# Performance work log

Hardware: AMD Instinct MI355X
Metric: run time of the kernel (lower is better)

## Reference

```python
import jax, jax.numpy as jnp
import numpy as np

N = 50000      # nodes
E = 800000     # edges
T = 3          # npass
ED = 64        # embedding_dim
NS = 23        # nshifts (arange(0.8, 3.0+1e-5, 0.1))
MD = NS + ED   # message_dim = 87
H = 200        # hidden width (hardcoded in module)
NMOL = 2048    # number of molecules (segments for final scatter)
RD = ED * (T + 1)  # readout input dim = 256
EPS = 1e-5

SHIFTS = jnp.asarray(np.arange(0.8, 3.0 + 1e-5, 0.1, dtype=np.float32))  # [23]


def setup_inputs() -> dict:
    key = jax.random.key(0)
    ks = jax.random.split(key, 32)
    inp = {
        'z_i': jax.random.randint(ks[0], (N,), 0, 10),
        'edge_index': jax.random.randint(ks[1], (2, E), 0, N),
        'dist_ij': jax.random.uniform(ks[2], (E, 1), dtype=jnp.float32) * 2.2 + 0.8,
        'mol_ind': jnp.sort(jax.random.randint(ks[3], (N,), 0, NMOL)),
        'emb': jax.random.normal(ks[4], (10, ED), dtype=jnp.float32),
        # per-pass update MLP params, stacked over T
        'up_bn_g': jnp.ones((T, MD), jnp.float32),
        'up_bn_b': jnp.zeros((T, MD), jnp.float32),
        'up_w1': jax.random.normal(ks[5], (T, MD, H), jnp.float32) * 0.05,
        'up_b1': jnp.zeros((T, H), jnp.float32),
        'up_w2': jax.random.normal(ks[6], (T, H, H), jnp.float32) * 0.05,
        'up_b2': jnp.zeros((T, H), jnp.float32),
        'up_w3': jax.random.normal(ks[7], (T, H, H), jnp.float32) * 0.05,
        'up_b3': jnp.zeros((T, H), jnp.float32),
        'up_w4': jax.random.normal(ks[8], (T, H, ED), jnp.float32) * 0.05,
        'up_b4': jnp.zeros((T, ED), jnp.float32),
        # readout MLP params
        'ro_bn_g': jnp.ones((RD,), jnp.float32),
        'ro_bn_b': jnp.zeros((RD,), jnp.float32),
        'ro_w1': jax.random.normal(ks[9], (RD, H), jnp.float32) * 0.05,
        'ro_b1': jnp.zeros((H,), jnp.float32),
        'ro_w2': jax.random.normal(ks[10], (H, H), jnp.float32) * 0.05,
        'ro_b2': jnp.zeros((H,), jnp.float32),
        'ro_w3': jax.random.normal(ks[11], (H, H), jnp.float32) * 0.05,
        'ro_b3': jnp.zeros((H,), jnp.float32),
        'ro_w4': jax.random.normal(ks[12], (H, 1), jnp.float32) * 0.05,
        'ro_b4': jnp.zeros((1,), jnp.float32),  # bias filled to 0 in __init__
    }
    return inp


def batchnorm(x, g, b):
    # BatchNorm1d in training mode: batch statistics, biased variance
    mu = jnp.mean(x, axis=0)
    var = jnp.mean(jnp.square(x - mu), axis=0)
    return (x - mu) * jax.lax.rsqrt(var + EPS) * g + b


def mlp(x, g, b, w1, b1, w2, b2, w3, b3, w4, b4):
    x = batchnorm(x, g, b)
    x = jax.nn.relu(x @ w1 + b1)
    x = jax.nn.relu(x @ w2 + b2)
    x = jax.nn.relu(x @ w3 + b3)
    return x @ w4 + b4


def reference(z_i, edge_index, dist_ij, mol_ind, emb,
              up_bn_g, up_bn_b, up_w1, up_b1, up_w2, up_b2, up_w3, up_b3, up_w4, up_b4,
              ro_bn_g, ro_bn_b, ro_w1, ro_b1, ro_w2, ro_b2, ro_w3, ro_b3, ro_w4, ro_b4):
    e_source, e_sink = edge_index[0], edge_index[1]
    rbf_ij = jnp.exp(-jnp.square(dist_ij - SHIFTS[None, :]))  # [E, NS]
    x_i = emb[z_i]                                            # [N, ED]
    x_list = [x_i]
    for t in range(T):
        m_ij = jnp.concatenate([rbf_ij, x_i[e_sink]], axis=1)  # [E, MD] gather
        m_i = jax.ops.segment_sum(m_ij, e_source, num_segments=N)  # scatter-sum
        x_i = x_i + 0.1 * mlp(m_i, up_bn_g[t], up_bn_b[t],
                              up_w1[t], up_b1[t], up_w2[t], up_b2[t],
                              up_w3[t], up_b3[t], up_w4[t], up_b4[t])
        x_list.append(x_i)
    x_all = jnp.concatenate(x_list, axis=1)  # [N, RD]
    y_i = mlp(x_all, ro_bn_g, ro_bn_b, ro_w1, ro_b1, ro_w2, ro_b2, ro_w3, ro_b3, ro_w4, ro_b4)
    y = jax.ops.segment_sum(y_i, mol_ind, num_segments=NMOL)  # [NMOL, 1]
    return y
```

## Files before the change

kernel.cpp:

```cpp
#include <hip/hip_runtime.h>
#include <hip/hip_bf16.h>
#include <type_traits>

#define NN 50000
#define NP 50048
#define EE 800000
#define TT 3
#define ED 64
#define NS 23
#define MD 87
#define HH 200
#define NMOL 2048
#define RD 256

#define SW 216
#define NPB2 512
#define SNB ((NN + 255) / 256)

typedef __attribute__((ext_vector_type(8))) short short8b;
typedef __attribute__((ext_vector_type(4))) float f32x4;

__device__ __forceinline__ unsigned short f2bf(float f) {
  unsigned u = __float_as_uint(f);
  return (unsigned short)((u + 0x7fffu + ((u >> 16) & 1u)) >> 16);
}
__device__ __forceinline__ float ubf2f(unsigned short h) {
  return __uint_as_float(((unsigned)h) << 16);
}
__device__ __forceinline__ float bfp2f(unsigned p) {
  return __uint_as_float(p << 16) + __uint_as_float(p & 0xffff0000u);
}
__device__ __forceinline__ unsigned packsplit(float v) {
  unsigned short h = f2bf(v);
  unsigned short l = f2bf(v - ubf2f(h));
  return (unsigned)h | ((unsigned)l << 16);
}

__device__ __forceinline__ void gl2lds16(const short* g, short* l) {
  __builtin_amdgcn_global_load_lds(
      (const __attribute__((address_space(1))) unsigned int*)g,
      (__attribute__((address_space(3))) unsigned int*)l, 16, 0, 0);
}

struct WD { const float* src; short* dst; int K, N, Kpad, Npad, T; };
struct WDs { WD d[5]; };

__global__ __launch_bounds__(256) void wprep_kernel(WDs W) {
  WD w = W.d[blockIdx.y];
  int KB = w.Kpad >> 5, NT = w.Npad >> 4;
  int per = w.Npad * w.Kpad;
  int total = w.T * per;
  for (int idx = blockIdx.x * 256 + threadIdx.x; idx < total; idx += gridDim.x * 256) {
    int t = idx / per;
    int r = idx - t * per;
    int e = r & 7, lane = (r >> 3) & 63;
    int blk = r >> 9;
    int kb = blk % KB, tile = blk / KB;
    int ln = lane & 15, quad = lane >> 4;
    int n = tile * 16 + ln, k = kb * 32 + quad * 8 + e;
    float v = 0.f;
    if (k < w.K && n < w.N) v = w.src[((size_t)t * w.K + k) * w.N + n];
    unsigned short h = f2bf(v);
    unsigned short l = f2bf(v - ubf2f(h));
    size_t base = ((size_t)(t * NT + tile) * KB + kb) * 1024;
    w.dst[base + lane * 8 + e] = (short)h;
    w.dst[base + 512 + lane * 8 + e] = (short)l;
  }
}

__global__ __launch_bounds__(256) void wscale_kernel(const float* __restrict__ wsrc,
                                                     const float* __restrict__ na,
                                                     const float* __restrict__ nb,
                                                     const float* __restrict__ bsrc,
                                                     int K, int Kpad,
                                                     short* __restrict__ wsp,
                                                     float* __restrict__ bc) {
  int n = blockIdx.x;
  int k = threadIdx.x;
  int KB = Kpad >> 5;
  int tile = n >> 4, ln = n & 15;
  float contrib = 0.f;
  if (k < Kpad) {
    float v = 0.f;
    if (n < HH && k < K) {
      float w = wsrc[(size_t)k * HH + n];
      v = na[k] * w;
      contrib = nb[k] * w;
    }
    unsigned short h = f2bf(v);
    unsigned short l = f2bf(v - ubf2f(h));
    int kb = k >> 5, quad = (k & 31) >> 3, e = k & 7;
    int lane = quad * 16 + ln;
    size_t base = ((size_t)tile * KB + kb) * 1024;
    wsp[base + lane * 8 + e] = (short)h;
    wsp[base + 512 + lane * 8 + e] = (short)l;
  }
  __shared__ float sh[256];
  sh[k] = contrib;
  __syncthreads();
  for (int off = 128; off > 0; off >>= 1) {
    if (k < off) sh[k] += sh[k + off];
    __syncthreads();
  }
  if (k == 0) bc[n] = (n < HH ? bsrc[n] : 0.f) + sh[0];
}

__global__ __launch_bounds__(256) void emb_kernel(const int* __restrict__ z,
                                                  const float* __restrict__ emb,
                                                  unsigned* __restrict__ xp,
                                                  short* __restrict__ xq,
                                                  short* __restrict__ xqs) {
  int idx = blockIdx.x * 256 + threadIdx.x;
  if (idx >= NN * ED) return;
  int i = idx >> 6, d = idx & 63;
  unsigned pk = packsplit(emb[z[i] * ED + d]);
  xp[(size_t)i * RD + d] = pk;
  short h = (short)(pk & 0xffffu);
  xq[(size_t)i * RD + d] = h;
  xqs[(size_t)i * ED + d] = h;
}

__global__ __launch_bounds__(256) void hist_kernel(const int* __restrict__ src,
                                                   int* __restrict__ deg) {
  int e = blockIdx.x * 256 + threadIdx.x;
  if (e < EE) atomicAdd(&deg[src[e]], 1);
}

__global__ __launch_bounds__(256) void scanA_kernel(const int* __restrict__ deg,
                                                    int* __restrict__ Psum) {
  int i = blockIdx.x * 256 + threadIdx.x;
  int v = (i < NN) ? deg[i] : 0;
#pragma unroll
  for (int off = 32; off > 0; off >>= 1) v += __shfl_down(v, off, 64);
  __shared__ int ws[4];
  if ((threadIdx.x & 63) == 0) ws[threadIdx.x >> 6] = v;
  __syncthreads();
  if (threadIdx.x == 0) Psum[blockIdx.x] = ws[0] + ws[1] + ws[2] + ws[3];
}

__global__ __launch_bounds__(256) void scanB_kernel(const int* __restrict__ Psum,
                                                    int* __restrict__ Poff) {
  __shared__ int sh[256];
  int t = threadIdx.x;
  int v = (t < SNB) ? Psum[t] : 0;
  sh[t] = v;
  __syncthreads();
  for (int off = 1; off < 256; off <<= 1) {
    int u = (t >= off) ? sh[t - off] : 0;
    __syncthreads();
    sh[t] += u;
    __syncthreads();
  }
  if (t < SNB) Poff[t] = sh[t] - v;
}

__global__ __launch_bounds__(256) void scanC_kernel(const int* __restrict__ deg,
                                                    const int* __restrict__ Poff,
                                                    int* __restrict__ offs,
                                                    int* __restrict__ cursor) {
  __shared__ int sh[256];
  int t = threadIdx.x;
  int i = blockIdx.x * 256 + t;
  int v = (i < NN) ? deg[i] : 0;
  sh[t] = v;
  __syncthreads();
  for (int off = 1; off < 256; off <<= 1) {
    int u = (t >= off) ? sh[t - off] : 0;
    __syncthreads();
    sh[t] += u;
    __syncthreads();
  }
  int excl = Poff[blockIdx.x] + sh[t] - v;
  if (i < NN) {
    offs[i] = excl;
    cursor[i] = excl;
    if (i == NN - 1) offs[NN] = excl + v;
  }
}

__global__ __launch_bounds__(256) void scatter_kernel(const int* __restrict__ src,
                                                      const int* __restrict__ snk,
                                                      const float* __restrict__ dist,
                                                      int* __restrict__ cursor,
                                                      int* __restrict__ ssink,
                                                      float* __restrict__ sdist) {
  int e = blockIdx.x * 256 + threadIdx.x;
  if (e >= EE) return;
  int p = atomicAdd(&cursor[src[e]], 1);
  ssink[p] = snk[e];
  sdist[p] = dist[e];
}

template <bool RBF>
__global__ __launch_bounds__(256) void gather_kernel(const int* __restrict__ offs,
                                                     const int* __restrict__ ssink,
                                                     const float* __restrict__ sdist,
                                                     const short* __restrict__ xqs,
                                                     short* __restrict__ mh) {
  int node = blockIdx.x * 4 + (threadIdx.x >> 6);
  int lane = threadIdx.x & 63;
  if (node >= NN) return;
  float shift = (float)(0.8 + 0.1 * (double)lane);
  int e0 = offs[node], e1 = offs[node + 1];
  float ax0 = 0.f, ax1 = 0.f, ar0 = 0.f, ar1 = 0.f;
  int j = e0;
  for (; j + 4 <= e1; j += 4) {
    int s0 = ssink[j], s1 = ssink[j + 1], s2 = ssink[j + 2], s3 = ssink[j + 3];
    float x0 = ubf2f((unsigned short)xqs[(size_t)s0 * ED + lane]);
    float x1 = ubf2f((unsigned short)xqs[(size_t)s1 * ED + lane]);
    float x2 = ubf2f((unsigned short)xqs[(size_t)s2 * ED + lane]);
    float x3 = ubf2f((unsigned short)xqs[(size_t)s3 * ED + lane]);
    ax0 += x0 + x2;
    ax1 += x1 + x3;
    if (RBF && lane < NS) {
      float d0 = sdist[j], d1 = sdist[j + 1], d2 = sdist[j + 2], d3 = sdist[j + 3];
      float u0 = d0 - shift, u1 = d1 - shift, u2 = d2 - shift, u3 = d3 - shift;
      ar0 += __expf(-u0 * u0) + __expf(-u2 * u2);
      ar1 += __expf(-u1 * u1) + __expf(-u3 * u3);
    }
  }
  for (; j < e1; j++) {
    int s = ssink[j];
    ax0 += ubf2f((unsigned short)xqs[(size_t)s * ED + lane]);
    if (RBF && lane < NS) {
      float u = sdist[j] - shift;
      ar0 += __expf(-u * u);
    }
  }
  float accx = ax0 + ax1;
  if (RBF && lane < NS) mh[(size_t)node * 96 + lane] = (short)f2bf(ar0 + ar1);
  if (RBF && lane >= NS && lane < 32) mh[(size_t)node * 96 + 64 + lane] = 0;
  mh[(size_t)node * 96 + NS + lane] = (short)f2bf(accx);
}

template <int LD>
__global__ __launch_bounds__(256) void colstats_s16_kernel(const short* __restrict__ X,
                                                           float* __restrict__ P) {
  constexpr int CG = LD / 8;
  constexpr int RPB = 256 / CG;
  const int t = threadIdx.x;
  const int cg = t % CG, rin = t / CG;
  float s[8] = {0, 0, 0, 0, 0, 0, 0, 0}, q[8] = {0, 0, 0, 0, 0, 0, 0, 0};
  if (rin < RPB) {
    for (int r = blockIdx.x * RPB + rin; r < NN; r += gridDim.x * RPB) {
      union { uint4 v; short e[8]; } u;
      u.v = *(const uint4*)(X + (size_t)r * LD + cg * 8);
#pragma unroll
      for (int e = 0; e < 8; e++) {
        float f = ubf2f((unsigned short)u.e[e]);
        s[e] += f;
        q[e] += f * f;
      }
    }
  }
  __shared__ float sh[256][16];
#pragma unroll
  for (int e = 0; e < 8; e++) { sh[t][e] = s[e]; sh[t][8 + e] = q[e]; }
  __syncthreads();
  if (rin == 0) {
    for (int rr = 1; rr < RPB; rr++) {
      const float* o = sh[rr * CG + cg];
#pragma unroll
      for (int e = 0; e < 8; e++) { s[e] += o[e]; q[e] += o[8 + e]; }
    }
    float* Pb = P + blockIdx.x * 512;
#pragma unroll
    for (int e = 0; e < 8; e++) {
      Pb[cg * 8 + e] = s[e];
      Pb[256 + cg * 8 + e] = q[e];
    }
  }
}

__global__ __launch_bounds__(256) void bnfinal2_kernel(const float* __restrict__ P, int nblk,
                                                       const float* __restrict__ g,
                                                       const float* __restrict__ b, int ncols,
                                                       float* __restrict__ na,
                                                       float* __restrict__ nb) {
  int c = blockIdx.x;
  int t = threadIdx.x;
  float s = 0.f, q = 0.f;
  for (int i = t; i < nblk; i += 256) {
    s += P[i * 512 + c];
    q += P[i * 512 + 256 + c];
  }
#pragma unroll
  for (int off = 32; off > 0; off >>= 1) {
    s += __shfl_down(s, off, 64);
    q += __shfl_down(q, off, 64);
  }
  __shared__ float ws[4], wq[4];
  if ((t & 63) == 0) { ws[t >> 6] = s; wq[t >> 6] = q; }
  __syncthreads();
  if (t == 0) {
    s = ws[0] + ws[1] + ws[2] + ws[3];
    q = wq[0] + wq[1] + wq[2] + wq[3];
    if (c < ncols) {
      float mean = s / (float)NN;
      float var = q / (float)NN - mean * mean;
      float a = g[c] * rsqrtf(var + 1e-5f);
      na[c] = a;
      nb[c] = b[c] - mean * a;
    } else {
      na[c] = 0.f;
      nb[c] = 0.f;
    }
  }
}

template <bool READOUT>
__global__ __launch_bounds__(256, 3) void fused_kernel(
    const short* __restrict__ Agh,
    const short* __restrict__ W1p, const short* __restrict__ W2p,
    const short* __restrict__ W3p, const short* __restrict__ W4p,
    const float* __restrict__ b1, const float* __restrict__ b2,
    const float* __restrict__ b3, const float* __restrict__ b4,
    unsigned* __restrict__ xp, short* __restrict__ xq, short* __restrict__ xqs,
    int t, const float* __restrict__ w4ro, const int* __restrict__ mol,
    float* __restrict__ out) {
  __shared__ short act[64 * SW];
  __shared__ short bufW[2][13 * 512];
  constexpr int GLDA = READOUT ? RD : 96;
  constexpr int KB1 = READOUT ? 8 : 3;
  const int tid = threadIdx.x;
  const int wave = tid >> 6, lane = tid & 63, ln = lane & 15, quad = lane >> 4;
  const int q8 = quad * 8;
  const int bm = blockIdx.x * 64;

  f32x4 acc[4][4];
  const short8b zfrag = {0, 0, 0, 0, 0, 0, 0, 0};

  auto stage = [&](const short* __restrict__ Wp, int NT, int KB, int TERMS,
                   int s, int b) {
    int kb = (TERMS == 2) ? (s >> 1) : s;
    int pl = (TERMS == 2) ? ((s & 1) << 9) : 0;
#pragma unroll
    for (int j = 0; j < 4; j++) {
      int tile = wave + 4 * j;
      if (tile < NT)
        gl2lds16(Wp + (size_t)(tile * KB + kb) * 1024 + pl + lane * 8,
                 &bufW[b][tile * 512]);
    }
  };

  auto runloop = [&](const short* __restrict__ AG, const short* __restrict__ Wp,
                     int NT, int KB, int TERMS) {
    const int NSL = KB * TERMS;
#pragma unroll
    for (int j = 0; j < 4; j++)
#pragma unroll
      for (int i = 0; i < 4; i++) acc[j][i] = (f32x4){0.f, 0.f, 0.f, 0.f};
    for (int s = 0; s < NSL; ++s) {
      if (s + 1 < NSL) stage(Wp, NT, KB, TERMS, s + 1, (s + 1) & 1);
      int kb = (TERMS == 2) ? (s >> 1) : s;
      short8b a[4];
      if (AG) {
#pragma unroll
        for (int i = 0; i < 4; i++)
          a[i] = *(const short8b*)(AG + (size_t)(bm + i * 16 + ln) * GLDA +
                                   kb * 32 + q8);
      } else {
        int col = kb * 32 + q8;
#pragma unroll
        for (int i = 0; i < 4; i++)
          a[i] = (col < 208) ? *(const short8b*)(act + (i * 16 + ln) * SW + col)
                             : zfrag;
      }
      const short* bw = &bufW[s & 1][0];
#pragma unroll
      for (int j = 0; j < 4; j++) {
        int tile = wave + 4 * j;
        if (tile < NT) {
          short8b b = *(const short8b*)(bw + tile * 512 + lane * 8);
#pragma unroll
          for (int i = 0; i < 4; i++)
            acc[j][i] =
                __builtin_amdgcn_mfma_f32_16x16x32_bf16(a[i], b, acc[j][i], 0, 0, 0);
        }
      }
      __syncthreads();
    }
  };

  auto epi = [&](const float* __restrict__ bias) {
#pragma unroll
    for (int j = 0; j < 4; j++) {
      int tile = wave + 4 * j;
      if (tile < 13) {
        int colg = tile * 16 + ln;
        float bb = (colg < HH) ? bias[colg] : 0.f;
#pragma unroll
        for (int i = 0; i < 4; i++)
#pragma unroll
          for (int r = 0; r < 4; r++)
            act[(i * 16 + quad * 4 + r) * SW + colg] =
                (short)f2bf(fmaxf(acc[j][i][r] + bb, 0.f));
      }
    }
  };

  stage(W1p, 13, KB1, 2, 0, 0);
  __syncthreads();
  runloop(Agh, W1p, 13, KB1, 2);
  stage(W2p, 13, 7, 1, 0, 0);
  epi(b1);
  __syncthreads();

  runloop(nullptr, W2p, 13, 7, 1);
  stage(W3p, 13, 7, 1, 0, 0);
  epi(b2);
  __syncthreads();

  runloop(nullptr, W3p, 13, 7, 1);

  if constexpr (!READOUT) {
    stage(W4p, 4, 7, 2, 0, 0);
    epi(b3);
    __syncthreads();
    runloop(nullptr, W4p, 4, 7, 2);
    int colg = wave * 16 + ln;
    float bb = b4[colg];
#pragma unroll
    for (int i = 0; i < 4; i++)
#pragma unroll
      for (int r = 0; r < 4; r++) {
        int grow = bm + i * 16 + quad * 4 + r;
        if (grow < NN) {
          size_t base = (size_t)grow * RD;
          float oldv = bfp2f(xp[base + (size_t)t * ED + colg]);
          unsigned pk = packsplit(oldv + 0.1f * (acc[0][i][r] + bb));
          xp[base + (size_t)(t + 1) * ED + colg] = pk;
          short h = (short)(pk & 0xffffu);
          xq[base + (size_t)(t + 1) * ED + colg] = h;
          xqs[(size_t)(t + 1) * NN * ED + (size_t)grow * ED + colg] = h;
        }
      }
  } else {
    epi(b3);
    __syncthreads();
    int row = tid >> 2;
    float s = 0.f;
    for (int c = (tid & 3); c < HH; c += 4)
      s += ubf2f((unsigned short)act[row * SW + c]) * w4ro[c];
    s += __shfl_xor(s, 1, 64);
    s += __shfl_xor(s, 2, 64);
    int grow = bm + row;
    if ((tid & 3) == 0 && grow < NN) atomicAdd(&out[mol[grow]], s + b4[0]);
  }
}

extern "C" void kernel_launch(void* const* d_in, const int* in_sizes, int n_in,
                              void* d_out, int out_size, void* d_ws, size_t ws_size,
                              hipStream_t stream) {
  const int* z_i = (const int*)d_in[0];
  const int* e_src = (const int*)d_in[1];
  const int* e_snk = ((const int*)d_in[1]) + EE;
  const float* dist = (const float*)d_in[2];
  const int* mol = (const int*)d_in[3];
  const float* emb = (const float*)d_in[4];
  const float* up_bn_g = (const float*)d_in[5];
  const float* up_bn_b = (const float*)d_in[6];
  const float* up_w1 = (const float*)d_in[7];
  const float* up_b1 = (const float*)d_in[8];
  const float* up_w2 = (const float*)d_in[9];
  const float* up_b2 = (const float*)d_in[10];
  const float* up_w3 = (const float*)d_in[11];
  const float* up_b3 = (const float*)d_in[12];
  const float* up_w4 = (const float*)d_in[13];
  const float* up_b4 = (const float*)d_in[14];
  const float* ro_bn_g = (const float*)d_in[15];
  const float* ro_bn_b = (const float*)d_in[16];
  const float* ro_w1 = (const float*)d_in[17];
  const float* ro_b1 = (const float*)d_in[18];
  const float* ro_w2 = (const float*)d_in[19];
  const float* ro_b2 = (const float*)d_in[20];
  const float* ro_w3 = (const float*)d_in[21];
  const float* ro_b3 = (const float*)d_in[22];
  const float* ro_w4 = (const float*)d_in[23];
  const float* ro_b4 = (const float*)d_in[24];
  float* out = (float*)d_out;

  char* p = (char*)d_ws;
  auto alloc = [&](size_t bytes) {
    void* r = (void*)p;
    p += (bytes + 255) & ~(size_t)255;
    return r;
  };
  unsigned* x_p = (unsigned*)alloc((size_t)NN * RD * 4);
  short* x_q = (short*)alloc((size_t)NP * RD * 2);
  short* x_qs = (short*)alloc((size_t)(TT + 1) * NN * ED * 2);
  short* mh = (short*)alloc((size_t)NP * 96 * 2);
  int* ssink = (int*)alloc((size_t)EE * 4);
  float* sdist = (float*)alloc((size_t)EE * 4);
  int* offs = (int*)alloc((size_t)(NN + 1) * 4);
  int* deg = (int*)alloc((size_t)NN * 4);
  int* cursor = (int*)alloc((size_t)NN * 4);
  int* Psum = (int*)alloc((size_t)SNB * 4);
  int* Poff = (int*)alloc((size_t)SNB * 4);
  float* P = (float*)alloc((size_t)NPB2 * 512 * 4);
  float* na = (float*)alloc(256 * 4);
  float* nb = (float*)alloc(256 * 4);
  float* b1c = (float*)alloc(208 * 4);
  short* w1sp = (short*)alloc((size_t)13 * 3 * 1024 * 2);
  short* r1sp = (short*)alloc((size_t)13 * 8 * 1024 * 2);
  short* w2p = (short*)alloc((size_t)TT * 13 * 7 * 1024 * 2);
  short* w3p = (short*)alloc((size_t)TT * 13 * 7 * 1024 * 2);
  short* w4p = (short*)alloc((size_t)TT * 4 * 7 * 1024 * 2);
  short* r2p = (short*)alloc((size_t)13 * 7 * 1024 * 2);
  short* r3p = (short*)alloc((size_t)13 * 7 * 1024 * 2);

  hipMemsetAsync(deg, 0, (size_t)NN * 4, stream);
  hipMemsetAsync(out, 0, (size_t)NMOL * 4, stream);

  WDs descs;
  descs.d[0] = {up_w2, w2p, HH, HH, 224, 208, TT};
  descs.d[1] = {up_w3, w3p, HH, HH, 224, 208, TT};
  descs.d[2] = {up_w4, w4p, HH, ED, 224, 64, TT};
  descs.d[3] = {ro_w2, r2p, HH, HH, 224, 208, 1};
  descs.d[4] = {ro_w3, r3p, HH, HH, 224, 208, 1};
  wprep_kernel<<<dim3(546, 5), 256, 0, stream>>>(descs);

  emb_kernel<<<(NN * ED + 255) / 256, 256, 0, stream>>>(z_i, emb, x_p, x_q, x_qs);
  hist_kernel<<<(EE + 255) / 256, 256, 0, stream>>>(e_src, deg);
  scanA_kernel<<<SNB, 256, 0, stream>>>(deg, Psum);
  scanB_kernel<<<1, 256, 0, stream>>>(Psum, Poff);
  scanC_kernel<<<SNB, 256, 0, stream>>>(deg, Poff, offs, cursor);
  scatter_kernel<<<(EE + 255) / 256, 256, 0, stream>>>(e_src, e_snk, dist, cursor, ssink, sdist);

  const int gM = NP / 64;

  for (int t = 0; t < TT; t++) {
    if (t == 0)
      gather_kernel<true><<<(NN + 3) / 4, 256, 0, stream>>>(
          offs, ssink, sdist, x_qs, mh);
    else
      gather_kernel<false><<<(NN + 3) / 4, 256, 0, stream>>>(
          offs, ssink, sdist, x_qs + (size_t)t * NN * ED, mh);
    colstats_s16_kernel<96><<<NPB2, 256, 0, stream>>>(mh, P);
    bnfinal2_kernel<<<256, 256, 0, stream>>>(P, NPB2, up_bn_g + t * MD, up_bn_b + t * MD, MD,
                                             na, nb);
    wscale_kernel<<<208, 256, 0, stream>>>(up_w1 + (size_t)t * MD * HH, na, nb,
                                           up_b1 + t * HH, MD, 96, w1sp, b1c);
    fused_kernel<false><<<gM, 256, 0, stream>>>(
        mh, w1sp,
        w2p + (size_t)t * 13 * 7 * 1024, w3p + (size_t)t * 13 * 7 * 1024,
        w4p + (size_t)t * 4 * 7 * 1024,
        b1c, up_b2 + t * HH, up_b3 + t * HH, up_b4 + t * ED,
        x_p, x_q, x_qs, t, nullptr, nullptr, nullptr);
  }

  colstats_s16_kernel<256><<<NPB2, 256, 0, stream>>>(x_q, P);
  bnfinal2_kernel<<<256, 256, 0, stream>>>(P, NPB2, ro_bn_g, ro_bn_b, RD, na, nb);
  wscale_kernel<<<208, 256, 0, stream>>>(ro_w1, na, nb, ro_b1, RD, 256, r1sp, b1c);
  fused_kernel<true><<<gM, 256, 0, stream>>>(
      x_q, r1sp, r2p, r3p, nullptr,
      b1c, ro_b2, ro_b3, ro_b4,
      nullptr, nullptr, nullptr, 0, ro_w4, mol, out);

  (void)in_sizes; (void)n_in; (void)out_size; (void)ws_size;
}
```

Measured before the change: 632.2 us.

## Hold MLP weight fragments in registers instead of double-buffered LDS staging

Each layer's packed weight fragments are now loaded directly from global memory into a per-thread register array, replacing the LDS double-buffer fed by global_load_lds and its per-k-step barriers. The fully unrolled MFMA loop reads B operands from registers, and only a few explicit barriers remain around the activation epilogues. This trades higher register pressure (launch bounds lowered from 3 to 2 blocks per CU) and redundant global weight loads per block for fewer synchronisations and less LDS traffic. Weight loads for the next layer are issued before the epilogue so they overlap with it.

```diff
diff --git a/kernel.cpp b/kernel.cpp
--- a/kernel.cpp
+++ b/kernel.cpp
@@ -20,6 +20,8 @@
 typedef __attribute__((ext_vector_type(8))) short short8b;
 typedef __attribute__((ext_vector_type(4))) float f32x4;
 
+template <int V> using ic = std::integral_constant<int, V>;
+
 __device__ __forceinline__ unsigned short f2bf(float f) {
   unsigned u = __float_as_uint(f);
   return (unsigned short)((u + 0x7fffu + ((u >> 16) & 1u)) >> 16);
@@ -34,12 +36,6 @@
   unsigned short h = f2bf(v);
   unsigned short l = f2bf(v - ubf2f(h));
   return (unsigned)h | ((unsigned)l << 16);
-}
-
-__device__ __forceinline__ void gl2lds16(const short* g, short* l) {
-  __builtin_amdgcn_global_load_lds(
-      (const __attribute__((address_space(1))) unsigned int*)g,
-      (__attribute__((address_space(3))) unsigned int*)l, 16, 0, 0);
 }
 
 struct WD { const float* src; short* dst; int K, N, Kpad, Npad, T; };
@@ -309,7 +305,7 @@
 }
 
 template <bool READOUT>
-__global__ __launch_bounds__(256, 3) void fused_kernel(
+__global__ __launch_bounds__(256, 2) void fused_kernel(
     const short* __restrict__ Agh,
     const short* __restrict__ W1p, const short* __restrict__ W2p,
     const short* __restrict__ W3p, const short* __restrict__ W4p,
@@ -319,66 +315,77 @@
     int t, const float* __restrict__ w4ro, const int* __restrict__ mol,
     float* __restrict__ out) {
   __shared__ short act[64 * SW];
-  __shared__ short bufW[2][13 * 512];
   constexpr int GLDA = READOUT ? RD : 96;
   constexpr int KB1 = READOUT ? 8 : 3;
+  constexpr int NB = READOUT ? 32 : 28;
   const int tid = threadIdx.x;
   const int wave = tid >> 6, lane = tid & 63, ln = lane & 15, quad = lane >> 4;
   const int q8 = quad * 8;
   const int bm = blockIdx.x * 64;
 
+  *(unsigned*)(act + (tid >> 2) * SW + 208 + (tid & 3) * 2) = 0u;
+
   f32x4 acc[4][4];
+  short8b Breg[NB];
   const short8b zfrag = {0, 0, 0, 0, 0, 0, 0, 0};
 
-  auto stage = [&](const short* __restrict__ Wp, int NT, int KB, int TERMS,
-                   int s, int b) {
-    int kb = (TERMS == 2) ? (s >> 1) : s;
-    int pl = (TERMS == 2) ? ((s & 1) << 9) : 0;
+  auto loadB = [&](auto slt, auto tmt, auto ntt, const short* __restrict__ Wp,
+                   int KBfull, int kb0) {
+    constexpr int SL = decltype(slt)::value;
+    constexpr int TM = decltype(tmt)::value;
+    constexpr int NT = decltype(ntt)::value;
 #pragma unroll
     for (int j = 0; j < 4; j++) {
       int tile = wave + 4 * j;
-      if (tile < NT)
-        gl2lds16(Wp + (size_t)(tile * KB + kb) * 1024 + pl + lane * 8,
-                 &bufW[b][tile * 512]);
+      if (tile < NT) {
+#pragma unroll
+        for (int s = 0; s < SL; s++) {
+          int kb = kb0 + ((TM == 2) ? (s >> 1) : s);
+          int pl = (TM == 2) ? ((s & 1) << 9) : 0;
+          Breg[j * SL + s] = *(const short8b*)(
+              Wp + (size_t)(tile * KBfull + kb) * 1024 + pl + lane * 8);
+        }
+      }
     }
   };
 
-  auto runloop = [&](const short* __restrict__ AG, const short* __restrict__ Wp,
-                     int NT, int KB, int TERMS) {
-    const int NSL = KB * TERMS;
-#pragma unroll
-    for (int j = 0; j < 4; j++)
-#pragma unroll
-      for (int i = 0; i < 4; i++) acc[j][i] = (f32x4){0.f, 0.f, 0.f, 0.f};
-    for (int s = 0; s < NSL; ++s) {
-      if (s + 1 < NSL) stage(Wp, NT, KB, TERMS, s + 1, (s + 1) & 1);
-      int kb = (TERMS == 2) ? (s >> 1) : s;
+  auto mfmaloop = [&](auto slt, auto tmt, auto ntt, auto gat, auto rstt, int kb0) {
+    constexpr int SL = decltype(slt)::value;
+    constexpr int TM = decltype(tmt)::value;
+    constexpr int NT = decltype(ntt)::value;
+    constexpr bool GA = decltype(gat)::value;
+    constexpr bool RST = decltype(rstt)::value;
+    constexpr int KB = SL / TM;
+    if constexpr (RST) {
+#pragma unroll
+      for (int j = 0; j < 4; j++)
+#pragma unroll
+        for (int i = 0; i < 4; i++) acc[j][i] = (f32x4){0.f, 0.f, 0.f, 0.f};
+    }
+#pragma unroll
+    for (int kb = 0; kb < KB; kb++) {
+      int col = (kb0 + kb) * 32 + q8;
       short8b a[4];
-      if (AG) {
-#pragma unroll
-        for (int i = 0; i < 4; i++)
-          a[i] = *(const short8b*)(AG + (size_t)(bm + i * 16 + ln) * GLDA +
-                                   kb * 32 + q8);
-      } else {
-        int col = kb * 32 + q8;
-#pragma unroll
-        for (int i = 0; i < 4; i++)
-          a[i] = (col < 208) ? *(const short8b*)(act + (i * 16 + ln) * SW + col)
+#pragma unroll
+      for (int i = 0; i < 4; i++) {
+        if constexpr (GA)
+          a[i] = *(const short8b*)(Agh + (size_t)(bm + i * 16 + ln) * GLDA + col);
+        else
+          a[i] = (col < 216) ? *(const short8b*)(act + (i * 16 + ln) * SW + col)
                              : zfrag;
       }
-      const short* bw = &bufW[s & 1][0];
-#pragma unroll
-      for (int j = 0; j < 4; j++) {
-        int tile = wave + 4 * j;
-        if (tile < NT) {
-          short8b b = *(const short8b*)(bw + tile * 512 + lane * 8);
-#pragma unroll
-          for (int i = 0; i < 4; i++)
-            acc[j][i] =
-                __builtin_amdgcn_mfma_f32_16x16x32_bf16(a[i], b, acc[j][i], 0, 0, 0);
+#pragma unroll
+      for (int s2 = 0; s2 < TM; s2++)
+#pragma unroll
+        for (int j = 0; j < 4; j++) {
+          int tile = wave + 4 * j;
+          if (tile < NT) {
+#pragma unroll
+            for (int i = 0; i < 4; i++)
+              acc[j][i] = __builtin_amdgcn_mfma_f32_16x16x32_bf16(
+                  a[i], Breg[j * SL + kb * TM + s2], acc[j][i], 0, 0, 0);
+          }
         }
-      }
-      __syncthreads();
     }
   };
 
@@ -399,25 +406,49 @@
     }
   };
 
-  stage(W1p, 13, KB1, 2, 0, 0);
-  __syncthreads();
-  runloop(Agh, W1p, 13, KB1, 2);
-  stage(W2p, 13, 7, 1, 0, 0);
+  auto bar = [] {
+    __builtin_amdgcn_sched_barrier(0);
+    __builtin_amdgcn_s_barrier();
+    __builtin_amdgcn_sched_barrier(0);
+  };
+  auto lgkmbar = [] {
+    asm volatile("s_waitcnt lgkmcnt(0)" ::: "memory");
+    __builtin_amdgcn_sched_barrier(0);
+    __builtin_amdgcn_s_barrier();
+    __builtin_amdgcn_sched_barrier(0);
+  };
+
+  using T = std::true_type;
+  using F = std::false_type;
+
+  if constexpr (!READOUT) {
+    loadB(ic<6>{}, ic<2>{}, ic<13>{}, W1p, KB1, 0);
+    mfmaloop(ic<6>{}, ic<2>{}, ic<13>{}, T{}, T{}, 0);
+  } else {
+    loadB(ic<8>{}, ic<2>{}, ic<13>{}, W1p, KB1, 0);
+    mfmaloop(ic<8>{}, ic<2>{}, ic<13>{}, T{}, T{}, 0);
+    loadB(ic<8>{}, ic<2>{}, ic<13>{}, W1p, KB1, 4);
+    mfmaloop(ic<8>{}, ic<2>{}, ic<13>{}, T{}, F{}, 4);
+  }
+  loadB(ic<7>{}, ic<1>{}, ic<13>{}, W2p, 7, 0);
   epi(b1);
-  __syncthreads();
-
-  runloop(nullptr, W2p, 13, 7, 1);
-  stage(W3p, 13, 7, 1, 0, 0);
+  lgkmbar();
+
+  mfmaloop(ic<7>{}, ic<1>{}, ic<13>{}, F{}, T{}, 0);
+  loadB(ic<7>{}, ic<1>{}, ic<13>{}, W3p, 7, 0);
+  bar();
   epi(b2);
-  __syncthreads();
-
-  runloop(nullptr, W3p, 13, 7, 1);
+  lgkmbar();
+
+  mfmaloop(ic<7>{}, ic<1>{}, ic<13>{}, F{}, T{}, 0);
+  if constexpr (!READOUT)
+    loadB(ic<14>{}, ic<2>{}, ic<4>{}, W4p, 7, 0);
+  bar();
+  epi(b3);
+  lgkmbar();
 
   if constexpr (!READOUT) {
-    stage(W4p, 4, 7, 2, 0, 0);
-    epi(b3);
-    __syncthreads();
-    runloop(nullptr, W4p, 4, 7, 2);
+    mfmaloop(ic<14>{}, ic<2>{}, ic<4>{}, F{}, T{}, 0);
     int colg = wave * 16 + ln;
     float bb = b4[colg];
 #pragma unroll
@@ -436,8 +467,6 @@
         }
       }
   } else {
-    epi(b3);
-    __syncthreads();
     int row = tid >> 2;
     float s = 0.f;
     for (int c = (tid & 3); c < HH; c += 4)
```

After: 553.0 us. 12.5% less time.
